# Kernel tuning notes

Hardware: AMD Instinct MI355X
Metric: run time of the kernel (lower is better)

The kernel has to match this reference:

```python
import jax, jax.numpy as jnp
import numpy as np

B, C, H, W = 32, 1024, 48, 24
P = 3            # num_parts
IC = C // 8      # inter_channels for position attention
PH = H // P      # part height


def setup_inputs() -> dict:
    key = jax.random.key(0)
    ks = jax.random.split(key, 16)
    s = 0.02
    return {
        "x": jax.random.normal(ks[0], (B, C, H, W), jnp.float32),
        "modality": jax.random.randint(ks[1], (B,), 0, 2),
        # per-part 1x1 conv weights (stacked over parts)
        "Wq": jax.random.normal(ks[2], (P, IC, C), jnp.float32) * s,
        "bq": jnp.zeros((P, IC), jnp.float32),
        "Wk": jax.random.normal(ks[3], (P, IC, C), jnp.float32) * s,
        "bk": jnp.zeros((P, IC), jnp.float32),
        "Wv": jax.random.normal(ks[4], (P, C, C), jnp.float32) * s,
        "bv": jnp.zeros((P, C), jnp.float32),
        # gamma residual scales (torch inits to 0; random so output differs from x)
        "gamma_pa": jax.random.normal(ks[5], (P,), jnp.float32) * 0.1,
        "gamma_ca": jax.random.normal(ks[6], (P,), jnp.float32) * 0.1,
        # modality gate: Linear(1,64) -> ReLU -> Linear(64,P) -> Sigmoid
        "gW1": jax.random.normal(ks[7], (64, 1), jnp.float32) * 0.01,
        "gb1": jnp.zeros((64,), jnp.float32),
        "gW2": jax.random.normal(ks[8], (P, 64), jnp.float32) * 0.01,
        "gb2": jnp.zeros((P,), jnp.float32),
    }


def _part_dual_attn(part, Wq, bq, Wk, bk, Wv, bv, g_pa, g_ca):
    # part: [B, C, ph, W]
    b, c, ph, w = part.shape
    n = ph * w
    xf = part.reshape(b, c, n)  # [B,C,N]
    # --- Position attention (PAM) ---
    q = jnp.einsum('oc,bcn->bno', Wq, xf) + bq            # [B,N,IC]
    k = jnp.einsum('oc,bcn->bon', Wk, xf) + bk[:, None]   # [B,IC,N]
    attn = jax.nn.softmax(jnp.einsum('bno,bom->bnm', q, k), axis=-1)  # [B,N,N]
    v = jnp.einsum('oc,bcn->bon', Wv, xf) + bv[:, None]   # [B,C,N]
    pa = jnp.einsum('bcn,bmn->bcm', v, attn).reshape(part.shape)
    pa = g_pa * pa + part
    # --- Channel attention (CAM) with max-shifted softmax ---
    e = jnp.einsum('bcn,bdn->bcd', xf, xf)                # [B,C,C]
    e = jnp.max(e, axis=-1, keepdims=True) - e
    ca_attn = jax.nn.softmax(e, axis=-1)
    ca = jnp.einsum('bcd,bdn->bcn', ca_attn, xf).reshape(part.shape)
    ca = g_ca * ca + part
    return pa + ca


def reference(x, modality, Wq, bq, Wk, bk, Wv, bv, gamma_pa, gamma_ca, gW1, gb1, gW2, gb2):
    b = x.shape[0]
    # modality gate -> per-sample per-part blend weights [B,P]
    m = modality.astype(jnp.float32)[:, None]
    h = jax.nn.relu(m @ gW1.T + gb1)
    w_gate = jax.nn.sigmoid(h @ gW2.T + gb2)              # [B,P]
    # split into P horizontal parts: [P,B,C,ph,W]
    parts = x.reshape(b, C, P, PH, W).transpose(2, 0, 1, 3, 4)
    part_outs = jax.vmap(_part_dual_attn)(parts, Wq, bq, Wk, bk, Wv, bv, gamma_pa, gamma_ca)
    wp = w_gate.T[:, :, None, None, None]                 # [P,B,1,1,1]
    blended = parts * (1.0 - wp) + part_outs * wp         # [P,B,C,ph,W]
    return blended.transpose(1, 2, 0, 3, 4).reshape(b, C, H, W)
```

## Files before the change

kernel.cpp:

```cpp
#include <hip/hip_runtime.h>
#include <hip/hip_bf16.h>
#include <cstdint>

constexpr int kB  = 32;
constexpr int kC  = 1024;
constexpr int kH  = 48;
constexpr int kW  = 24;
constexpr int kP  = 3;
constexpr int kPH = 16;
constexpr int kN  = kPH * kW;
constexpr int kHW = kH * kW;
constexpr int64_t kCHW = (int64_t)kC * kHW;

typedef __attribute__((ext_vector_type(8))) short short8b;
typedef __attribute__((ext_vector_type(4))) float f32x4;

__device__ __forceinline__ void gl_lds16(const void* g, void* l) {
    __builtin_amdgcn_global_load_lds(
        (const __attribute__((address_space(1))) void*)g,
        (__attribute__((address_space(3))) void*)l, 16, 0, 0);
}

__device__ __forceinline__ void swz_block(int& bx, int& by, int& bz) {
    const int gx = gridDim.x, gy = gridDim.y, gz = gridDim.z;
    if ((gz & 7) == 0) {
        const int tpp = gx * gy;
        const int L   = (blockIdx.z * gy + blockIdx.y) * gx + blockIdx.x;
        const int xcd = L & 7;
        const int idx = L >> 3;
        const int ppx = gz >> 3;
        const int pairL = idx / tpp;
        const int tile  = idx - pairL * tpp;
        bz = xcd * ppx + pairL;
        by = tile / gx;
        bx = tile - by * gx;
    } else {
        bx = blockIdx.x; by = blockIdx.y; bz = blockIdx.z;
    }
}

#define WAIT12()      asm volatile("s_waitcnt vmcnt(12)" ::: "memory")
#define WAIT8()       asm volatile("s_waitcnt vmcnt(8)" ::: "memory")
#define WAIT6()       asm volatile("s_waitcnt vmcnt(6)" ::: "memory")
#define WAIT0()       asm volatile("s_waitcnt vmcnt(0)" ::: "memory")
#define RAW_BARRIER() asm volatile("s_barrier" ::: "memory")
#define SFENCE()      __builtin_amdgcn_sched_barrier(0)

__global__ void gate_kernel(const int* __restrict__ modality,
                            const float* __restrict__ gW1, const float* __restrict__ gb1,
                            const float* __restrict__ gW2, const float* __restrict__ gb2,
                            const float* __restrict__ gpa, const float* __restrict__ gca,
                            const float* __restrict__ bq, const float* __restrict__ bk,
                            float* __restrict__ wg, float* __restrict__ cpa,
                            float* __restrict__ cca, float* __restrict__ bqk)
{
    const int t = threadIdx.x;
    if (t < 768) {
        const int p = t >> 8, o = t & 255;
        bqk[t] = (o < 128) ? bq[p * 128 + o] : bk[p * 128 + (o - 128)];
    }
    if (t < kB * kP) {
        const int b = t / kP, p = t % kP;
        const float m = (float)modality[b];
        float acc = gb2[p];
        #pragma unroll
        for (int j = 0; j < 64; ++j) {
            float h = fmaxf(fmaf(m, gW1[j], gb1[j]), 0.0f);
            acc = fmaf(gW2[p * 64 + j], h, acc);
        }
        const float w = 1.0f / (1.0f + __expf(-acc));
        wg[t]  = w;
        cpa[t] = w * gpa[p];
        cca[t] = w * gca[p];
    }
}

__global__ __launch_bounds__(256)
void wcast_kernel(const float* __restrict__ Wq, const float* __restrict__ Wk,
                  const float* __restrict__ Wv,
                  __hip_bfloat16* __restrict__ Wqkb, __hip_bfloat16* __restrict__ Wvb)
{
    const int64_t i = (int64_t)blockIdx.x * 256 + threadIdx.x;
    if (i < 196608) {
        const int64_t e = i * 4;
        const int p = (int)(e / 262144);
        const int rem = (int)(e % 262144);
        const int o = rem / 1024, c = rem % 1024;
        const float* s = (o < 128) ? (Wq + (int64_t)p * 131072 + (int64_t)o * 1024 + c)
                                   : (Wk + (int64_t)p * 131072 + (int64_t)(o - 128) * 1024 + c);
        float4 v = *(const float4*)s;
        __hip_bfloat16* d = Wqkb + e;
        d[0] = __float2bfloat16(v.x); d[1] = __float2bfloat16(v.y);
        d[2] = __float2bfloat16(v.z); d[3] = __float2bfloat16(v.w);
    } else if (i < 196608 + 786432) {
        const int64_t e = (i - 196608) * 4;
        float4 v = *(const float4*)(Wv + e);
        __hip_bfloat16* d = Wvb + e;
        d[0] = __float2bfloat16(v.x); d[1] = __float2bfloat16(v.y);
        d[2] = __float2bfloat16(v.z); d[3] = __float2bfloat16(v.w);
    }
}

__global__ void zeroz_kernel(float* __restrict__ Z)
{
    Z[(int64_t)blockIdx.x * 1024 + threadIdx.x] = 0.0f;
}

__global__ __launch_bounds__(256)
void cast_tr_kernel(const float* __restrict__ x,
                    __hip_bfloat16* __restrict__ xfb,
                    __hip_bfloat16* __restrict__ xfT)
{
    int bx, by, bz;
    swz_block(bx, by, bz);
    const int j = bz;
    const int bb = j / kP, pp = j % kP;
    const float* src = x + (int64_t)bb * kCHW + pp * kN;
    const int c0 = bx * 32, n0 = by * 128;
    __shared__ float tile[32][129];
    const int tx = threadIdx.x & 31, ty = threadIdx.x >> 5;
    #pragma unroll
    for (int r = 0; r < 4; ++r) {
        const int cl = ty * 4 + r;
        const int c  = c0 + cl;
        float4 v = *(const float4*)(src + (int64_t)c * kHW + n0 + tx * 4);
        __hip_bfloat16 h0 = __float2bfloat16(v.x), h1 = __float2bfloat16(v.y);
        __hip_bfloat16 h2 = __float2bfloat16(v.z), h3 = __float2bfloat16(v.w);
        ushort4 hv;
        hv.x = *(ushort*)&h0; hv.y = *(ushort*)&h1;
        hv.z = *(ushort*)&h2; hv.w = *(ushort*)&h3;
        *(ushort4*)((ushort*)xfb + (int64_t)j * 393216 + (int64_t)c * kN + n0 + tx * 4) = hv;
        tile[cl][tx * 4 + 0] = v.x; tile[cl][tx * 4 + 1] = v.y;
        tile[cl][tx * 4 + 2] = v.z; tile[cl][tx * 4 + 3] = v.w;
    }
    __syncthreads();
    const int cc = (threadIdx.x & 15) * 2;
    const int nr = threadIdx.x >> 4;
    #pragma unroll
    for (int r = 0; r < 8; ++r) {
        const int nl = r * 16 + nr;
        __hip_bfloat16 h0 = __float2bfloat16(tile[cc][nl]);
        __hip_bfloat16 h1 = __float2bfloat16(tile[cc + 1][nl]);
        ushort2 h2; h2.x = *(ushort*)&h0; h2.y = *(ushort*)&h1;
        *(ushort2*)((ushort*)xfT + (int64_t)j * 393216 + (int64_t)(n0 + nl) * kC + c0 + cc) = h2;
    }
}

template<int BIAS>
__global__ __launch_bounds__(256, 2)
void mm_kernel(const __hip_bfloat16* __restrict__ A0, int64_t aSB, int64_t aSP, int lda,
               const __hip_bfloat16* __restrict__ B0, int64_t bSB, int64_t bSP, int ldb,
               __hip_bfloat16* __restrict__ C0, int64_t cSB, int64_t cSP, int ldc,
               const float* __restrict__ bias0, int biasSP, int K)
{
    __shared__ char lds[65536];

    int bx, by, bz;
    swz_block(bx, by, bz);
    const int j = bz, bb = j / kP, pp = j % kP;
    const char* Ab = (const char*)(A0 + (int64_t)bb * aSB + (int64_t)pp * aSP);
    const char* Bb = (const char*)(B0 + (int64_t)bb * bSB + (int64_t)pp * bSP);
    const int m0 = bx * 128, n0 = by * 128;
    const int t = threadIdx.x, lane = t & 63, wv = t >> 6;
    const int wm = (wv & 1) * 64, wn = (wv >> 1) * 64;
    const size_t ldab = (size_t)lda * 2, ldbb = (size_t)ldb * 2;

    const int rr   = wv * 8 + (lane >> 3);
    const int gsrc = ((lane & 7) ^ (lane >> 3)) * 16;
    const int lrow = (wv * 8 + (lane >> 3)) * 128 + (lane & 7) * 16;

    auto STAGE = [&](int buf, int k0) {
        const char* Asrc = Ab + (size_t)(m0 + rr) * ldab + (size_t)k0 * 2 + gsrc;
        const char* Bsrc = Bb + (size_t)(n0 + rr) * ldbb + (size_t)k0 * 2 + gsrc;
        char* As = lds + buf * 32768;
        char* Bs = As + 16384;
        #pragma unroll
        for (int i = 0; i < 4; ++i) {
            gl_lds16(Asrc + (size_t)i * 32 * ldab, As + i * 4096 + lrow);
            gl_lds16(Bsrc + (size_t)i * 32 * ldbb, Bs + i * 4096 + lrow);
        }
    };

    f32x4 acc[4][4];
    #pragma unroll
    for (int a = 0; a < 4; ++a)
        #pragma unroll
        for (int b = 0; b < 4; ++b) acc[a][b] = (f32x4){0.f, 0.f, 0.f, 0.f};

    const int nk = K >> 6;
    STAGE(0, 0);
    int cur = 0;
    for (int k = 0; k < nk; ++k) {
        if (k + 1 < nk) { STAGE(cur ^ 1, (k + 1) << 6); WAIT8(); }
        else            { WAIT0(); }
        SFENCE();
        RAW_BARRIER();
        const char* As = lds + cur * 32768;
        const char* Bs = As + 16384;
        #pragma unroll
        for (int kk = 0; kk < 2; ++kk) {
            const int gpos = ((kk * 4 + (lane >> 4)) ^ (lane & 7)) * 16;
            short8b af[4], bf[4];
            #pragma unroll
            for (int f = 0; f < 4; ++f) {
                af[f] = *(const short8b*)(As + (wm + f * 16 + (lane & 15)) * 128 + gpos);
                bf[f] = *(const short8b*)(Bs + (wn + f * 16 + (lane & 15)) * 128 + gpos);
            }
            #pragma unroll
            for (int fm = 0; fm < 4; ++fm)
                #pragma unroll
                for (int fn = 0; fn < 4; ++fn)
                    acc[fm][fn] = __builtin_amdgcn_mfma_f32_16x16x32_bf16(
                        af[fm], bf[fn], acc[fm][fn], 0, 0, 0);
        }
        RAW_BARRIER();
        cur ^= 1;
    }

    __hip_bfloat16* Cm = C0 + (int64_t)bb * cSB + (int64_t)pp * cSP;
    #pragma unroll
    for (int fn = 0; fn < 4; ++fn) {
        const int col = n0 + wn + fn * 16 + (lane & 15);
        const float cb = (BIAS == 2) ? bias0[pp * biasSP + col] : 0.0f;
        #pragma unroll
        for (int fm = 0; fm < 4; ++fm)
            #pragma unroll
            for (int jr = 0; jr < 4; ++jr) {
                const int row = m0 + wm + fm * 16 + (lane >> 4) * 4 + jr;
                Cm[(int64_t)row * ldc + col] = __float2bfloat16(acc[fm][fn][jr] + cb);
            }
    }
}

__global__ __launch_bounds__(256, 2)
void ecam_kernel(const __hip_bfloat16* __restrict__ xfb,
                 __hip_bfloat16* __restrict__ eb,
                 float* __restrict__ Z)
{
    __shared__ char lds[65536];

    int bx, by, bz;
    swz_block(bx, by, bz);
    const int j = bz;
    int bi = 0;
    while ((bi + 1) * (bi + 2) / 2 <= bx) ++bi;
    const int bj = bx - bi * (bi + 1) / 2;
    const char* Ab = (const char*)(xfb + (int64_t)j * 393216);
    const int m0 = bi * 128, n0 = bj * 128;
    const int t = threadIdx.x, lane = t & 63, wv = t >> 6;
    const int wm = (wv & 1) * 64, wn = (wv >> 1) * 64;
    constexpr size_t ldab = 768;

    const int rr   = wv * 8 + (lane >> 3);
    const int gsrc = ((lane & 7) ^ (lane >> 3)) * 16;
    const int lrow = (wv * 8 + (lane >> 3)) * 128 + (lane & 7) * 16;

    auto STAGE = [&](int buf, int k0) {
        const char* Asrc = Ab + (size_t)(m0 + rr) * ldab + (size_t)k0 * 2 + gsrc;
        const char* Bsrc = Ab + (size_t)(n0 + rr) * ldab + (size_t)k0 * 2 + gsrc;
        char* As = lds + buf * 32768;
        char* Bs = As + 16384;
        #pragma unroll
        for (int i = 0; i < 4; ++i) {
            gl_lds16(Asrc + (size_t)i * 32 * ldab, As + i * 4096 + lrow);
            gl_lds16(Bsrc + (size_t)i * 32 * ldab, Bs + i * 4096 + lrow);
        }
    };

    f32x4 acc[4][4];
    #pragma unroll
    for (int a = 0; a < 4; ++a)
        #pragma unroll
        for (int b = 0; b < 4; ++b) acc[a][b] = (f32x4){0.f, 0.f, 0.f, 0.f};

    STAGE(0, 0);
    int cur = 0;
    for (int k = 0; k < 6; ++k) {
        if (k + 1 < 6) { STAGE(cur ^ 1, (k + 1) << 6); WAIT8(); }
        else           { WAIT0(); }
        SFENCE();
        RAW_BARRIER();
        const char* As = lds + cur * 32768;
        const char* Bs = As + 16384;
        #pragma unroll
        for (int kk = 0; kk < 2; ++kk) {
            const int gpos = ((kk * 4 + (lane >> 4)) ^ (lane & 7)) * 16;
            short8b af[4], bf[4];
            #pragma unroll
            for (int f = 0; f < 4; ++f) {
                af[f] = *(const short8b*)(As + (wm + f * 16 + (lane & 15)) * 128 + gpos);
                bf[f] = *(const short8b*)(Bs + (wn + f * 16 + (lane & 15)) * 128 + gpos);
            }
            #pragma unroll
            for (int fm = 0; fm < 4; ++fm)
                #pragma unroll
                for (int fn = 0; fn < 4; ++fn)
                    acc[fm][fn] = __builtin_amdgcn_mfma_f32_16x16x32_bf16(
                        af[fm], bf[fn], acc[fm][fn], 0, 0, 0);
        }
        RAW_BARRIER();
        cur ^= 1;
    }

    #pragma unroll
    for (int fm = 0; fm < 4; ++fm)
        #pragma unroll
        for (int fn = 0; fn < 4; ++fn)
            #pragma unroll
            for (int jr = 0; jr < 4; ++jr)
                acc[fm][fn][jr] = __expf(-60.f - acc[fm][fn][jr]);

    __hip_bfloat16* Cm = eb + (int64_t)j * 1048576;
    float* Zp = Z + (int64_t)j * 1024;

    #pragma unroll
    for (int fm = 0; fm < 4; ++fm)
        #pragma unroll
        for (int jr = 0; jr < 4; ++jr) {
            const int row = m0 + wm + fm * 16 + (lane >> 4) * 4 + jr;
            float v = 0.f;
            #pragma unroll
            for (int fn = 0; fn < 4; ++fn) {
                const int col = n0 + wn + fn * 16 + (lane & 15);
                Cm[(int64_t)row * 1024 + col] = __float2bfloat16(acc[fm][fn][jr]);
                v += acc[fm][fn][jr];
            }
            v += __shfl_xor(v, 1);
            v += __shfl_xor(v, 2);
            v += __shfl_xor(v, 4);
            v += __shfl_xor(v, 8);
            if ((lane & 15) == 0) atomicAdd(Zp + row, v);
        }

    if (bi != bj) {
        #pragma unroll
        for (int fn = 0; fn < 4; ++fn) {
            const int col = n0 + wn + fn * 16 + (lane & 15);
            float v2 = 0.f;
            #pragma unroll
            for (int fm = 0; fm < 4; ++fm) {
                const int row0 = m0 + wm + fm * 16 + (lane >> 4) * 4;
                __hip_bfloat16 h0 = __float2bfloat16(acc[fm][fn][0]);
                __hip_bfloat16 h1 = __float2bfloat16(acc[fm][fn][1]);
                __hip_bfloat16 h2 = __float2bfloat16(acc[fm][fn][2]);
                __hip_bfloat16 h3 = __float2bfloat16(acc[fm][fn][3]);
                ushort4 w4;
                w4.x = *(ushort*)&h0; w4.y = *(ushort*)&h1;
                w4.z = *(ushort*)&h2; w4.w = *(ushort*)&h3;
                *(ushort4*)((ushort*)Cm + (int64_t)col * 1024 + row0) = w4;
                v2 += (acc[fm][fn][0] + acc[fm][fn][1]) +
                      (acc[fm][fn][2] + acc[fm][fn][3]);
            }
            v2 += __shfl_xor(v2, 16);
            v2 += __shfl_xor(v2, 32);
            if ((lane >> 4) == 0) atomicAdd(Zp + col, v2);
        }
    }
}

__global__ __launch_bounds__(256, 2)
void ep_cam_kernel(const __hip_bfloat16* __restrict__ Wvb,
                   const __hip_bfloat16* __restrict__ yTb,
                   const __hip_bfloat16* __restrict__ eb,
                   const __hip_bfloat16* __restrict__ xfT,
                   const float* __restrict__ Z,
                   const float* __restrict__ x,
                   float* __restrict__ out,
                   const float* __restrict__ wg,
                   const float* __restrict__ cpa,
                   const float* __restrict__ cca,
                   const float* __restrict__ bv)
{
    extern __shared__ char lds[];

    int bx, by, bz;
    swz_block(bx, by, bz);
    const int j = bz, bb = j / kP, pp = j % kP;
    const int m0 = bx * 256, n0 = by * 128;
    const int t = threadIdx.x, lane = t & 63, wv = t >> 6;
    const int wm = (wv & 1) * 128, wn = (wv >> 1) * 64;

    const int rr   = t >> 2;
    const int gsrc = ((t & 3) ^ ((t >> 3) & 3)) * 16;

    const char* AbW = (const char*)(Wvb + (int64_t)pp * 1048576);
    const char* AbE = (const char*)(eb  + (int64_t)j  * 1048576);
    const char* BbY = (const char*)(yTb + (int64_t)j * 393216);
    const char* BbX = (const char*)(xfT + (int64_t)j * 393216);

    auto STAGE = [&](int buf, int g) {
        const char* A = (g < 32) ? AbE : AbW;
        const char* B = (g < 32) ? BbX : BbY;
        const size_t k0b = (size_t)(g & 31) * 64;
        const char* Asrc = A + (size_t)(m0 + rr) * 2048 + k0b + gsrc;
        const char* Bsrc = B + (size_t)(n0 + rr) * 2048 + k0b + gsrc;
        char* As = lds + (size_t)buf * 24576;
        char* Bs = As + 16384;
        #pragma unroll
        for (int i = 0; i < 4; ++i)
            gl_lds16(Asrc + (size_t)i * 64 * 2048, As + i * 4096 + t * 16);
        #pragma unroll
        for (int i = 0; i < 2; ++i)
            gl_lds16(Bsrc + (size_t)i * 64 * 2048, Bs + i * 4096 + t * 16);
    };

    const float cfc = cca[j];
    const float* Zp = Z + (int64_t)j * 1024;
    f32x4 zsc[8];
    #pragma unroll
    for (int fm = 0; fm < 8; ++fm)
        #pragma unroll
        for (int jr = 0; jr < 4; ++jr) {
            const int row = m0 + wm + fm * 16 + (lane >> 4) * 4 + jr;
            zsc[fm][jr] = cfc / Zp[row];
        }

    f32x4 acc[8][4];
    #pragma unroll
    for (int a = 0; a < 8; ++a)
        #pragma unroll
        for (int b = 0; b < 4; ++b) acc[a][b] = (f32x4){0.f, 0.f, 0.f, 0.f};

    const int gpos = ((lane >> 4) ^ ((lane >> 1) & 3)) * 16;

    STAGE(0, 0);
    STAGE(1, 1);
    int cur = 0;
    #pragma unroll 1
    for (int g = 0; g < 64; ++g) {
        if (g < 62) {
            int nb = cur + 2; if (nb >= 3) nb -= 3;
            STAGE(nb, g + 2);
            WAIT12();
        } else if (g == 62) { WAIT6(); }
        else                { WAIT0(); }
        SFENCE();
        RAW_BARRIER();
        if (g == 32) {
            #pragma unroll
            for (int fm = 0; fm < 8; ++fm)
                #pragma unroll
                for (int jr = 0; jr < 4; ++jr) {
                    const float zs = zsc[fm][jr];
                    #pragma unroll
                    for (int fn = 0; fn < 4; ++fn) acc[fm][fn][jr] *= zs;
                }
        }
        const char* As = lds + (size_t)cur * 24576;
        const char* Bs = As + 16384;
        short8b bf[4];
        #pragma unroll
        for (int f = 0; f < 4; ++f)
            bf[f] = *(const short8b*)(Bs + (wn + f * 16 + (lane & 15)) * 64 + gpos);
        {
            short8b af[4];
            #pragma unroll
            for (int f = 0; f < 4; ++f)
                af[f] = *(const short8b*)(As + (wm + f * 16 + (lane & 15)) * 64 + gpos);
            #pragma unroll
            for (int fm = 0; fm < 4; ++fm)
                #pragma unroll
                for (int fn = 0; fn < 4; ++fn)
                    acc[fm][fn] = __builtin_amdgcn_mfma_f32_16x16x32_bf16(
                        af[fm], bf[fn], acc[fm][fn], 0, 0, 0);
        }
        {
            short8b af[4];
            #pragma unroll
            for (int f = 0; f < 4; ++f)
                af[f] = *(const short8b*)(As + (wm + (f + 4) * 16 + (lane & 15)) * 64 + gpos);
            #pragma unroll
            for (int fm = 0; fm < 4; ++fm)
                #pragma unroll
                for (int fn = 0; fn < 4; ++fn)
                    acc[fm + 4][fn] = __builtin_amdgcn_mfma_f32_16x16x32_bf16(
                        af[fm], bf[fn], acc[fm + 4][fn], 0, 0, 0);
        }
        RAW_BARRIER();
        if (++cur == 3) cur = 0;
    }

    const float gsc = 1.0f + wg[j];
    const float cfp = cpa[j];
    const float* Xm = x   + (int64_t)bb * kCHW + pp * kN;
    float*       Om = out + (int64_t)bb * kCHW + pp * kN;
    #pragma unroll
    for (int fm = 0; fm < 8; ++fm)
        #pragma unroll
        for (int jr = 0; jr < 4; ++jr) {
            const int row = m0 + wm + fm * 16 + (lane >> 4) * 4 + jr;
            const float rb = cfp * bv[pp * 1024 + row];
            #pragma unroll
            for (int fn = 0; fn < 4; ++fn) {
                const int col = n0 + wn + fn * 16 + (lane & 15);
                const int64_t off = (int64_t)row * kHW + col;
                Om[off] = fmaf(gsc, Xm[off], acc[fm][fn][jr] + rb);
            }
        }
}

__global__ __launch_bounds__(256) void sm_pam(__hip_bfloat16* __restrict__ buf,
                                              const float* __restrict__ scale,
                                              int chPairs)
{
    const int R = blockIdx.x * 4 + (threadIdx.x >> 6);
    const int pair = R / kN, row = R % kN;
    __hip_bfloat16* rp = buf + (int64_t)pair * (kN * kN) + (int64_t)row * kN;
    const int t = threadIdx.x & 63;
    float v[6];
    float mx = -3.402823466e38f;
    #pragma unroll
    for (int r = 0; r < 6; ++r) {
        v[r] = __bfloat162float(rp[t + 64 * r]);
        mx = fmaxf(mx, v[r]);
    }
    #pragma unroll
    for (int off = 32; off > 0; off >>= 1) mx = fmaxf(mx, __shfl_xor(mx, off));
    float s = 0.0f;
    #pragma unroll
    for (int r = 0; r < 6; ++r) { v[r] = __expf(v[r] - mx); s += v[r]; }
    #pragma unroll
    for (int off = 32; off > 0; off >>= 1) s += __shfl_xor(s, off);
    const float inv = scale[pair] / s;
    #pragma unroll
    for (int r = 0; r < 6; ++r) rp[t + 64 * r] = __float2bfloat16(v[r] * inv);
}

extern "C" void kernel_launch(void* const* d_in, const int* in_sizes, int n_in,
                              void* d_out, int out_size, void* d_ws, size_t ws_size,
                              hipStream_t stream)
{
    const float* x   = (const float*)d_in[0];
    const int*   mod = (const int*)d_in[1];
    const float* Wq  = (const float*)d_in[2];
    const float* bq  = (const float*)d_in[3];
    const float* Wk  = (const float*)d_in[4];
    const float* bk  = (const float*)d_in[5];
    const float* Wv  = (const float*)d_in[6];
    const float* bv  = (const float*)d_in[7];
    const float* gpa = (const float*)d_in[8];
    const float* gca = (const float*)d_in[9];
    const float* gW1 = (const float*)d_in[10];
    const float* gb1 = (const float*)d_in[11];
    const float* gW2 = (const float*)d_in[12];
    const float* gb2 = (const float*)d_in[13];
    float* out = (float*)d_out;

    const int chList[6] = {96, 48, 24, 12, 6, 3};
    int CH = 3;
    for (int i = 0; i < 6; ++i) {
        size_t need = 7868544ull + (size_t)chList[i] * 4952064ull;
        if (need <= ws_size) { CH = chList[i]; break; }
    }
    const int NCHUNK = 96 / CH;

    char* ws = (char*)d_ws;
    __hip_bfloat16* Wqkb = (__hip_bfloat16*)(ws + 0);
    __hip_bfloat16* Wvb  = (__hip_bfloat16*)(ws + 1572864);
    float* bqk = (float*)(ws + 7864320);
    float* wg  = (float*)(ws + 7867392);
    float* cpa = (float*)(ws + 7867776);
    float* cca = (float*)(ws + 7868160);
    __hip_bfloat16* xfT   = (__hip_bfloat16*)(ws + 7868544);
    __hip_bfloat16* xfb   = xfT   + (int64_t)CH * 393216;
    __hip_bfloat16* qkT   = xfb   + (int64_t)CH * 393216;
    __hip_bfloat16* attnb = qkT   + (int64_t)CH * 98304;
    __hip_bfloat16* yTb   = attnb + (int64_t)CH * 147456;
    __hip_bfloat16* eb    = yTb   + (int64_t)CH * 393216;
    float*          Zbuf  = (float*)(eb + (int64_t)CH * 1048576);

    gate_kernel<<<1, 768, 0, stream>>>(mod, gW1, gb1, gW2, gb2, gpa, gca, bq, bk,
                                       wg, cpa, cca, bqk);
    wcast_kernel<<<3840, 256, 0, stream>>>(Wq, Wk, Wv, Wqkb, Wvb);

    for (int ch = 0; ch < NCHUNK; ++ch) {
        const int pair0 = ch * CH;
        const int b0 = pair0 / kP;
        const float* xc   = x   + (int64_t)b0 * kCHW;
        float*       outc = out + (int64_t)b0 * kCHW;

        cast_tr_kernel<<<dim3(32, 3, CH), 256, 0, stream>>>(xc, xfb, xfT);
        zeroz_kernel<<<CH, 1024, 0, stream>>>(Zbuf);

        mm_kernel<2><<<dim3(3, 2, CH), 256, 0, stream>>>(
            xfT, 3 * 393216, 393216, 1024,
            Wqkb, 0, 262144, 1024,
            qkT, 3 * 98304, 98304, 256,
            bqk, 256, 1024);
        mm_kernel<0><<<dim3(3, 3, CH), 256, 0, stream>>>(
            qkT, 3 * 98304, 98304, 256,
            qkT + 128, 3 * 98304, 98304, 256,
            attnb, 3 * 147456, 147456, 384,
            nullptr, 0, 128);
        sm_pam<<<CH * (kN / 4), 256, 0, stream>>>(attnb, cpa + pair0, CH);
        mm_kernel<0><<<dim3(3, 8, CH), 256, 0, stream>>>(
            attnb, 3 * 147456, 147456, 384,
            xfb, 3 * 393216, 393216, 384,
            yTb, 3 * 393216, 393216, 1024,
            nullptr, 0, 384);
        ecam_kernel<<<dim3(36, 1, CH), 256, 0, stream>>>(xfb, eb, Zbuf);
        ep_cam_kernel<<<dim3(4, 3, CH), 256, 73728, stream>>>(
            Wvb, yTb, eb, xfT, Zbuf, xc, outc,
            wg + pair0, cpa + pair0, cca + pair0, bv);
    }
}
```

Baseline: 549.6 us.

## Shrink ep_cam tile to 128x128 with 4-stage LDS ring and register double-buffering

```diff
diff --git a/kernel.cpp b/kernel.cpp
--- a/kernel.cpp
+++ b/kernel.cpp
@@ -39,9 +39,8 @@
     }
 }
 
-#define WAIT12()      asm volatile("s_waitcnt vmcnt(12)" ::: "memory")
 #define WAIT8()       asm volatile("s_waitcnt vmcnt(8)" ::: "memory")
-#define WAIT6()       asm volatile("s_waitcnt vmcnt(6)" ::: "memory")
+#define WAIT4()       asm volatile("s_waitcnt vmcnt(4)" ::: "memory")
 #define WAIT0()       asm volatile("s_waitcnt vmcnt(0)" ::: "memory")
 #define RAW_BARRIER() asm volatile("s_barrier" ::: "memory")
 #define SFENCE()      __builtin_amdgcn_sched_barrier(0)
@@ -371,14 +370,14 @@
                    const float* __restrict__ cca,
                    const float* __restrict__ bv)
 {
-    extern __shared__ char lds[];
+    __shared__ char lds[65536];
 
     int bx, by, bz;
     swz_block(bx, by, bz);
     const int j = bz, bb = j / kP, pp = j % kP;
-    const int m0 = bx * 256, n0 = by * 128;
+    const int m0 = bx * 128, n0 = by * 128;
     const int t = threadIdx.x, lane = t & 63, wv = t >> 6;
-    const int wm = (wv & 1) * 128, wn = (wv >> 1) * 64;
+    const int wm = (wv & 1) * 64, wn = (wv >> 1) * 64;
 
     const int rr   = t >> 2;
     const int gsrc = ((t & 3) ^ ((t >> 3) & 3)) * 16;
@@ -388,104 +387,108 @@
     const char* BbY = (const char*)(yTb + (int64_t)j * 393216);
     const char* BbX = (const char*)(xfT + (int64_t)j * 393216);
 
-    auto STAGE = [&](int buf, int g) {
-        const char* A = (g < 32) ? AbE : AbW;
-        const char* B = (g < 32) ? BbX : BbY;
-        const size_t k0b = (size_t)(g & 31) * 64;
+    auto STAGE = [&](int buf, int s) {
+        const char* A = (s < 32) ? AbE : AbW;
+        const char* B = (s < 32) ? BbX : BbY;
+        const size_t k0b = (size_t)(s & 31) * 64;
         const char* Asrc = A + (size_t)(m0 + rr) * 2048 + k0b + gsrc;
         const char* Bsrc = B + (size_t)(n0 + rr) * 2048 + k0b + gsrc;
-        char* As = lds + (size_t)buf * 24576;
-        char* Bs = As + 16384;
-        #pragma unroll
-        for (int i = 0; i < 4; ++i)
+        char* As = lds + buf * 16384;
+        char* Bs = As + 8192;
+        #pragma unroll
+        for (int i = 0; i < 2; ++i) {
             gl_lds16(Asrc + (size_t)i * 64 * 2048, As + i * 4096 + t * 16);
-        #pragma unroll
-        for (int i = 0; i < 2; ++i)
             gl_lds16(Bsrc + (size_t)i * 64 * 2048, Bs + i * 4096 + t * 16);
+        }
     };
 
     const float cfc = cca[j];
     const float* Zp = Z + (int64_t)j * 1024;
-    f32x4 zsc[8];
-    #pragma unroll
-    for (int fm = 0; fm < 8; ++fm)
+    float zsc[4][4];
+    #pragma unroll
+    for (int fm = 0; fm < 4; ++fm)
         #pragma unroll
         for (int jr = 0; jr < 4; ++jr) {
             const int row = m0 + wm + fm * 16 + (lane >> 4) * 4 + jr;
             zsc[fm][jr] = cfc / Zp[row];
         }
 
-    f32x4 acc[8][4];
-    #pragma unroll
-    for (int a = 0; a < 8; ++a)
+    f32x4 acc[4][4];
+    #pragma unroll
+    for (int a = 0; a < 4; ++a)
         #pragma unroll
         for (int b = 0; b < 4; ++b) acc[a][b] = (f32x4){0.f, 0.f, 0.f, 0.f};
 
     const int gpos = ((lane >> 4) ^ ((lane >> 1) & 3)) * 16;
 
-    STAGE(0, 0);
-    STAGE(1, 1);
-    int cur = 0;
+    short8b aA[4], bA[4], aB[4], bB[4];
+
+#define READF(BUFIDX, NA, NB)                                                 \
+    { const char* As_ = lds + (BUFIDX) * 16384;                               \
+      const char* Bs_ = As_ + 8192;                                           \
+      _Pragma("unroll")                                                       \
+      for (int f = 0; f < 4; ++f) {                                           \
+          NA[f] = *(const short8b*)(As_ + (wm + f * 16 + (lane & 15)) * 64 + gpos); \
+          NB[f] = *(const short8b*)(Bs_ + (wn + f * 16 + (lane & 15)) * 64 + gpos); \
+      } }
+
+#define MM16(CA, CB)                                                          \
+    _Pragma("unroll")                                                         \
+    for (int fm = 0; fm < 4; ++fm)                                            \
+        _Pragma("unroll")                                                     \
+        for (int fn = 0; fn < 4; ++fn)                                        \
+            acc[fm][fn] = __builtin_amdgcn_mfma_f32_16x16x32_bf16(            \
+                CA[fm], CB[fn], acc[fm][fn], 0, 0, 0);
+
+#define RESCALE()                                                             \
+    _Pragma("unroll")                                                         \
+    for (int fm = 0; fm < 4; ++fm)                                            \
+        _Pragma("unroll")                                                     \
+        for (int jr = 0; jr < 4; ++jr) {                                      \
+            const float zs_ = zsc[fm][jr];                                    \
+            _Pragma("unroll")                                                 \
+            for (int fn = 0; fn < 4; ++fn) acc[fm][fn][jr] *= zs_;            \
+        }
+
+#define STEP(G, CA, CB, NA, NB)                                               \
+    {                                                                         \
+        if ((G) < 61) STAGE(((G) + 3) & 3, (G) + 3);                          \
+        if ((G) < 61)      { WAIT8(); }                                       \
+        else if ((G)==61)  { WAIT4(); }                                       \
+        else               { WAIT0(); }                                       \
+        SFENCE();                                                             \
+        RAW_BARRIER();                                                        \
+        if ((G) == 32) { RESCALE(); }                                         \
+        READF(((G) + 1) & 3, NA, NB);                                         \
+        MM16(CA, CB);                                                         \
+    }
+
+    STAGE(0, 0); STAGE(1, 1); STAGE(2, 2);
+    WAIT8();
+    SFENCE();
+    RAW_BARRIER();
+    READF(0, aA, bA);
+
     #pragma unroll 1
-    for (int g = 0; g < 64; ++g) {
-        if (g < 62) {
-            int nb = cur + 2; if (nb >= 3) nb -= 3;
-            STAGE(nb, g + 2);
-            WAIT12();
-        } else if (g == 62) { WAIT6(); }
-        else                { WAIT0(); }
-        SFENCE();
-        RAW_BARRIER();
-        if (g == 32) {
-            #pragma unroll
-            for (int fm = 0; fm < 8; ++fm)
-                #pragma unroll
-                for (int jr = 0; jr < 4; ++jr) {
-                    const float zs = zsc[fm][jr];
-                    #pragma unroll
-                    for (int fn = 0; fn < 4; ++fn) acc[fm][fn][jr] *= zs;
-                }
-        }
-        const char* As = lds + (size_t)cur * 24576;
-        const char* Bs = As + 16384;
-        short8b bf[4];
-        #pragma unroll
-        for (int f = 0; f < 4; ++f)
-            bf[f] = *(const short8b*)(Bs + (wn + f * 16 + (lane & 15)) * 64 + gpos);
-        {
-            short8b af[4];
-            #pragma unroll
-            for (int f = 0; f < 4; ++f)
-                af[f] = *(const short8b*)(As + (wm + f * 16 + (lane & 15)) * 64 + gpos);
-            #pragma unroll
-            for (int fm = 0; fm < 4; ++fm)
-                #pragma unroll
-                for (int fn = 0; fn < 4; ++fn)
-                    acc[fm][fn] = __builtin_amdgcn_mfma_f32_16x16x32_bf16(
-                        af[fm], bf[fn], acc[fm][fn], 0, 0, 0);
-        }
-        {
-            short8b af[4];
-            #pragma unroll
-            for (int f = 0; f < 4; ++f)
-                af[f] = *(const short8b*)(As + (wm + (f + 4) * 16 + (lane & 15)) * 64 + gpos);
-            #pragma unroll
-            for (int fm = 0; fm < 4; ++fm)
-                #pragma unroll
-                for (int fn = 0; fn < 4; ++fn)
-                    acc[fm + 4][fn] = __builtin_amdgcn_mfma_f32_16x16x32_bf16(
-                        af[fm], bf[fn], acc[fm + 4][fn], 0, 0, 0);
-        }
-        RAW_BARRIER();
-        if (++cur == 3) cur = 0;
-    }
+    for (int gp = 0; gp < 31; ++gp) {
+        const int g = gp * 2;
+        STEP(g,     aA, bA, aB, bB);
+        STEP(g + 1, aB, bB, aA, bA);
+    }
+    STEP(62, aA, bA, aB, bB);
+    MM16(aB, bB);
+
+#undef READF
+#undef MM16
+#undef RESCALE
+#undef STEP
 
     const float gsc = 1.0f + wg[j];
     const float cfp = cpa[j];
     const float* Xm = x   + (int64_t)bb * kCHW + pp * kN;
     float*       Om = out + (int64_t)bb * kCHW + pp * kN;
     #pragma unroll
-    for (int fm = 0; fm < 8; ++fm)
+    for (int fm = 0; fm < 4; ++fm)
         #pragma unroll
         for (int jr = 0; jr < 4; ++jr) {
             const int row = m0 + wm + fm * 16 + (lane >> 4) * 4 + jr;
@@ -599,7 +602,7 @@
             yTb, 3 * 393216, 393216, 1024,
             nullptr, 0, 384);
         ecam_kernel<<<dim3(36, 1, CH), 256, 0, stream>>>(xfb, eb, Zbuf);
-        ep_cam_kernel<<<dim3(4, 3, CH), 256, 73728, stream>>>(
+        ep_cam_kernel<<<dim3(8, 3, CH), 256, 0, stream>>>(
             Wvb, yTb, eb, xfT, Zbuf, xc, outc,
             wg + pair0, cpa + pair0, cca + pair0, bv);
     }
```

After: 569.2 us. 1.04x slower.

## Drop multi-buffered LDS pipelining for single-buffer GEMMs with higher occupancy

Applied to the files above, without the earlier changes.

```diff
diff --git a/kernel.cpp b/kernel.cpp
--- a/kernel.cpp
+++ b/kernel.cpp
@@ -39,9 +39,6 @@
     }
 }
 
-#define WAIT12()      asm volatile("s_waitcnt vmcnt(12)" ::: "memory")
-#define WAIT8()       asm volatile("s_waitcnt vmcnt(8)" ::: "memory")
-#define WAIT6()       asm volatile("s_waitcnt vmcnt(6)" ::: "memory")
 #define WAIT0()       asm volatile("s_waitcnt vmcnt(0)" ::: "memory")
 #define RAW_BARRIER() asm volatile("s_barrier" ::: "memory")
 #define SFENCE()      __builtin_amdgcn_sched_barrier(0)
@@ -147,13 +144,13 @@
 }
 
 template<int BIAS>
-__global__ __launch_bounds__(256, 2)
+__global__ __launch_bounds__(256, 4)
 void mm_kernel(const __hip_bfloat16* __restrict__ A0, int64_t aSB, int64_t aSP, int lda,
                const __hip_bfloat16* __restrict__ B0, int64_t bSB, int64_t bSP, int ldb,
                __hip_bfloat16* __restrict__ C0, int64_t cSB, int64_t cSP, int ldc,
                const float* __restrict__ bias0, int biasSP, int K)
 {
-    __shared__ char lds[65536];
+    __shared__ char lds[32768];
 
     int bx, by, bz;
     swz_block(bx, by, bz);
@@ -169,10 +166,10 @@
     const int gsrc = ((lane & 7) ^ (lane >> 3)) * 16;
     const int lrow = (wv * 8 + (lane >> 3)) * 128 + (lane & 7) * 16;
 
-    auto STAGE = [&](int buf, int k0) {
+    auto STAGE = [&](int k0) {
         const char* Asrc = Ab + (size_t)(m0 + rr) * ldab + (size_t)k0 * 2 + gsrc;
         const char* Bsrc = Bb + (size_t)(n0 + rr) * ldbb + (size_t)k0 * 2 + gsrc;
-        char* As = lds + buf * 32768;
+        char* As = lds;
         char* Bs = As + 16384;
         #pragma unroll
         for (int i = 0; i < 4; ++i) {
@@ -188,14 +185,12 @@
         for (int b = 0; b < 4; ++b) acc[a][b] = (f32x4){0.f, 0.f, 0.f, 0.f};
 
     const int nk = K >> 6;
-    STAGE(0, 0);
-    int cur = 0;
     for (int k = 0; k < nk; ++k) {
-        if (k + 1 < nk) { STAGE(cur ^ 1, (k + 1) << 6); WAIT8(); }
-        else            { WAIT0(); }
+        STAGE(k << 6);
+        WAIT0();
         SFENCE();
         RAW_BARRIER();
-        const char* As = lds + cur * 32768;
+        const char* As = lds;
         const char* Bs = As + 16384;
         #pragma unroll
         for (int kk = 0; kk < 2; ++kk) {
@@ -214,7 +209,6 @@
                         af[fm], bf[fn], acc[fm][fn], 0, 0, 0);
         }
         RAW_BARRIER();
-        cur ^= 1;
     }
 
     __hip_bfloat16* Cm = C0 + (int64_t)bb * cSB + (int64_t)pp * cSP;
@@ -232,12 +226,12 @@
     }
 }
 
-__global__ __launch_bounds__(256, 2)
+__global__ __launch_bounds__(256, 4)
 void ecam_kernel(const __hip_bfloat16* __restrict__ xfb,
                  __hip_bfloat16* __restrict__ eb,
                  float* __restrict__ Z)
 {
-    __shared__ char lds[65536];
+    __shared__ char lds[32768];
 
     int bx, by, bz;
     swz_block(bx, by, bz);
@@ -255,10 +249,10 @@
     const int gsrc = ((lane & 7) ^ (lane >> 3)) * 16;
     const int lrow = (wv * 8 + (lane >> 3)) * 128 + (lane & 7) * 16;
 
-    auto STAGE = [&](int buf, int k0) {
+    auto STAGE = [&](int k0) {
         const char* Asrc = Ab + (size_t)(m0 + rr) * ldab + (size_t)k0 * 2 + gsrc;
         const char* Bsrc = Ab + (size_t)(n0 + rr) * ldab + (size_t)k0 * 2 + gsrc;
-        char* As = lds + buf * 32768;
+        char* As = lds;
         char* Bs = As + 16384;
         #pragma unroll
         for (int i = 0; i < 4; ++i) {
@@ -273,14 +267,12 @@
         #pragma unroll
         for (int b = 0; b < 4; ++b) acc[a][b] = (f32x4){0.f, 0.f, 0.f, 0.f};
 
-    STAGE(0, 0);
-    int cur = 0;
     for (int k = 0; k < 6; ++k) {
-        if (k + 1 < 6) { STAGE(cur ^ 1, (k + 1) << 6); WAIT8(); }
-        else           { WAIT0(); }
+        STAGE(k << 6);
+        WAIT0();
         SFENCE();
         RAW_BARRIER();
-        const char* As = lds + cur * 32768;
+        const char* As = lds;
         const char* Bs = As + 16384;
         #pragma unroll
         for (int kk = 0; kk < 2; ++kk) {
@@ -299,7 +291,6 @@
                         af[fm], bf[fn], acc[fm][fn], 0, 0, 0);
         }
         RAW_BARRIER();
-        cur ^= 1;
     }
 
     #pragma unroll
@@ -358,7 +349,7 @@
     }
 }
 
-__global__ __launch_bounds__(256, 2)
+__global__ __launch_bounds__(256, 4)
 void ep_cam_kernel(const __hip_bfloat16* __restrict__ Wvb,
                    const __hip_bfloat16* __restrict__ yTb,
                    const __hip_bfloat16* __restrict__ eb,
@@ -371,74 +362,65 @@
                    const float* __restrict__ cca,
                    const float* __restrict__ bv)
 {
-    extern __shared__ char lds[];
+    __shared__ char lds[32768];
 
     int bx, by, bz;
     swz_block(bx, by, bz);
     const int j = bz, bb = j / kP, pp = j % kP;
-    const int m0 = bx * 256, n0 = by * 128;
+    const int m0 = bx * 128, n0 = by * 128;
     const int t = threadIdx.x, lane = t & 63, wv = t >> 6;
-    const int wm = (wv & 1) * 128, wn = (wv >> 1) * 64;
-
-    const int rr   = t >> 2;
-    const int gsrc = ((t & 3) ^ ((t >> 3) & 3)) * 16;
+    const int wm = (wv & 1) * 64, wn = (wv >> 1) * 64;
+
+    const int rr   = wv * 8 + (lane >> 3);
+    const int gsrc = ((lane & 7) ^ (lane >> 3)) * 16;
+    const int lrow = (wv * 8 + (lane >> 3)) * 128 + (lane & 7) * 16;
 
     const char* AbW = (const char*)(Wvb + (int64_t)pp * 1048576);
     const char* AbE = (const char*)(eb  + (int64_t)j  * 1048576);
     const char* BbY = (const char*)(yTb + (int64_t)j * 393216);
     const char* BbX = (const char*)(xfT + (int64_t)j * 393216);
 
-    auto STAGE = [&](int buf, int g) {
-        const char* A = (g < 32) ? AbE : AbW;
-        const char* B = (g < 32) ? BbX : BbY;
-        const size_t k0b = (size_t)(g & 31) * 64;
+    auto STAGE = [&](int k) {
+        const char* A = (k < 16) ? AbE : AbW;
+        const char* B = (k < 16) ? BbX : BbY;
+        const size_t k0b = (size_t)(k & 15) * 128;
         const char* Asrc = A + (size_t)(m0 + rr) * 2048 + k0b + gsrc;
         const char* Bsrc = B + (size_t)(n0 + rr) * 2048 + k0b + gsrc;
-        char* As = lds + (size_t)buf * 24576;
+        char* As = lds;
         char* Bs = As + 16384;
         #pragma unroll
-        for (int i = 0; i < 4; ++i)
-            gl_lds16(Asrc + (size_t)i * 64 * 2048, As + i * 4096 + t * 16);
-        #pragma unroll
-        for (int i = 0; i < 2; ++i)
-            gl_lds16(Bsrc + (size_t)i * 64 * 2048, Bs + i * 4096 + t * 16);
+        for (int i = 0; i < 4; ++i) {
+            gl_lds16(Asrc + (size_t)i * 32 * 2048, As + i * 4096 + lrow);
+            gl_lds16(Bsrc + (size_t)i * 32 * 2048, Bs + i * 4096 + lrow);
+        }
     };
 
     const float cfc = cca[j];
     const float* Zp = Z + (int64_t)j * 1024;
-    f32x4 zsc[8];
-    #pragma unroll
-    for (int fm = 0; fm < 8; ++fm)
+    float zsc[4][4];
+    #pragma unroll
+    for (int fm = 0; fm < 4; ++fm)
         #pragma unroll
         for (int jr = 0; jr < 4; ++jr) {
             const int row = m0 + wm + fm * 16 + (lane >> 4) * 4 + jr;
             zsc[fm][jr] = cfc / Zp[row];
         }
 
-    f32x4 acc[8][4];
-    #pragma unroll
-    for (int a = 0; a < 8; ++a)
+    f32x4 acc[4][4];
+    #pragma unroll
+    for (int a = 0; a < 4; ++a)
         #pragma unroll
         for (int b = 0; b < 4; ++b) acc[a][b] = (f32x4){0.f, 0.f, 0.f, 0.f};
 
-    const int gpos = ((lane >> 4) ^ ((lane >> 1) & 3)) * 16;
-
-    STAGE(0, 0);
-    STAGE(1, 1);
-    int cur = 0;
     #pragma unroll 1
-    for (int g = 0; g < 64; ++g) {
-        if (g < 62) {
-            int nb = cur + 2; if (nb >= 3) nb -= 3;
-            STAGE(nb, g + 2);
-            WAIT12();
-        } else if (g == 62) { WAIT6(); }
-        else                { WAIT0(); }
+    for (int k = 0; k < 32; ++k) {
+        STAGE(k);
+        WAIT0();
         SFENCE();
         RAW_BARRIER();
-        if (g == 32) {
-            #pragma unroll
-            for (int fm = 0; fm < 8; ++fm)
+        if (k == 16) {
+            #pragma unroll
+            for (int fm = 0; fm < 4; ++fm)
                 #pragma unroll
                 for (int jr = 0; jr < 4; ++jr) {
                     const float zs = zsc[fm][jr];
@@ -446,17 +428,17 @@
                     for (int fn = 0; fn < 4; ++fn) acc[fm][fn][jr] *= zs;
                 }
         }
-        const char* As = lds + (size_t)cur * 24576;
+        const char* As = lds;
         const char* Bs = As + 16384;
-        short8b bf[4];
-        #pragma unroll
-        for (int f = 0; f < 4; ++f)
-            bf[f] = *(const short8b*)(Bs + (wn + f * 16 + (lane & 15)) * 64 + gpos);
-        {
-            short8b af[4];
-            #pragma unroll
-            for (int f = 0; f < 4; ++f)
-                af[f] = *(const short8b*)(As + (wm + f * 16 + (lane & 15)) * 64 + gpos);
+        #pragma unroll
+        for (int kk = 0; kk < 2; ++kk) {
+            const int gpos = ((kk * 4 + (lane >> 4)) ^ (lane & 7)) * 16;
+            short8b af[4], bf[4];
+            #pragma unroll
+            for (int f = 0; f < 4; ++f) {
+                af[f] = *(const short8b*)(As + (wm + f * 16 + (lane & 15)) * 128 + gpos);
+                bf[f] = *(const short8b*)(Bs + (wn + f * 16 + (lane & 15)) * 128 + gpos);
+            }
             #pragma unroll
             for (int fm = 0; fm < 4; ++fm)
                 #pragma unroll
@@ -464,20 +446,7 @@
                     acc[fm][fn] = __builtin_amdgcn_mfma_f32_16x16x32_bf16(
                         af[fm], bf[fn], acc[fm][fn], 0, 0, 0);
         }
-        {
-            short8b af[4];
-            #pragma unroll
-            for (int f = 0; f < 4; ++f)
-                af[f] = *(const short8b*)(As + (wm + (f + 4) * 16 + (lane & 15)) * 64 + gpos);
-            #pragma unroll
-            for (int fm = 0; fm < 4; ++fm)
-                #pragma unroll
-                for (int fn = 0; fn < 4; ++fn)
-                    acc[fm + 4][fn] = __builtin_amdgcn_mfma_f32_16x16x32_bf16(
-                        af[fm], bf[fn], acc[fm + 4][fn], 0, 0, 0);
-        }
         RAW_BARRIER();
-        if (++cur == 3) cur = 0;
     }
 
     const float gsc = 1.0f + wg[j];
@@ -485,7 +454,7 @@
     const float* Xm = x   + (int64_t)bb * kCHW + pp * kN;
     float*       Om = out + (int64_t)bb * kCHW + pp * kN;
     #pragma unroll
-    for (int fm = 0; fm < 8; ++fm)
+    for (int fm = 0; fm < 4; ++fm)
         #pragma unroll
         for (int jr = 0; jr < 4; ++jr) {
             const int row = m0 + wm + fm * 16 + (lane >> 4) * 4 + jr;
@@ -599,7 +568,7 @@
             yTb, 3 * 393216, 393216, 1024,
             nullptr, 0, 384);
         ecam_kernel<<<dim3(36, 1, CH), 256, 0, stream>>>(xfb, eb, Zbuf);
-        ep_cam_kernel<<<dim3(4, 3, CH), 256, 73728, stream>>>(
+        ep_cam_kernel<<<dim3(8, 3, CH), 256, 0, stream>>>(
             Wvb, yTb, eb, xfT, Zbuf, xc, outc,
             wg + pair0, cpa + pair0, cca + pair0, bv);
     }
```

Result: slower. 575.2 us (+4.7%).
